# Kernel optimization log

Hardware: AMD Instinct MI355X
Metric: run time of the kernel (lower is better)

Reference implementation:

```python
import jax, jax.numpy as jnp
import numpy as np

B, S, D, H = 16, 1024, 256, 8
DEPTH = D // H          # 32
H2 = H // 2             # 4 heads per branch
DH = D // 2             # 128 per-branch model dim


def setup_inputs() -> dict:
    key = jax.random.key(0)
    ks = jax.random.split(key, 20)
    f32 = jnp.float32
    q_ori = jax.random.normal(ks[0], (B, S, D), f32)
    k_ori = jax.random.normal(ks[1], (B, S, D), f32)
    v_ori = jax.random.normal(ks[2], (B, S, D), f32)
    mask = (jax.random.uniform(ks[3], (B, 1, 1, S)) < 0.1).astype(f32)
    # adjacency: sparse 0/1 graph structure
    adj = (jax.random.uniform(ks[4], (B, S, S)) < 0.05).astype(f32)
    # distance matrix: positive values, softmaxed inside the dist branch
    dist = jax.random.uniform(ks[5], (B, S, S), dtype=f32)

    def dense(k, din, dout):
        return jax.random.normal(k, (din, dout), f32) * 0.02

    params = {
        'Wq_dist': dense(ks[6], D, DH), 'bq_dist': jnp.zeros((DH,), f32),
        'Wk_dist': dense(ks[7], D, DH), 'bk_dist': jnp.zeros((DH,), f32),
        'Wv_dist': dense(ks[8], D, DH), 'bv_dist': jnp.zeros((DH,), f32),
        'Wq_adj': dense(ks[9], D, DH), 'bq_adj': jnp.zeros((DH,), f32),
        'Wk_adj': dense(ks[10], D, DH), 'bk_adj': jnp.zeros((DH,), f32),
        'Wv_adj': dense(ks[11], D, DH), 'bv_adj': jnp.zeros((DH,), f32),
        'Wo': dense(ks[12], D, D), 'bo': jnp.zeros((D,), f32),
    }
    return dict(v_ori=v_ori, k_ori=k_ori, q_ori=q_ori, mask=mask,
                adj=adj, dist=dist, **params)


def _split_heads(x):
    # (B, S, DH) -> (B, H2, S, DEPTH)
    b, s, _ = x.shape
    return x.reshape(b, s, H2, DEPTH).transpose(0, 2, 1, 3)


def _sdpa_AD(q, k, v, mask, adj=None, dist=None):
    neg = mask * (-1e9)                                   # (B,1,1,S)
    scale = 1.0 / jnp.sqrt(jnp.asarray(DEPTH, q.dtype))
    logits = jnp.einsum('bhqd,bhkd->bhqk', q, k) * scale + neg
    w = jax.nn.softmax(logits, axis=-1)                   # (B,H2,S,S)
    if adj is not None:
        w = w * adj[:, None]                              # multiplicative adjacency reweight
    if dist is not None:
        w = w * jax.nn.softmax(dist[:, None] + neg, axis=-1)
    out = jnp.einsum('bhqk,bhkd->bhqd', w, v)
    return out, w


def reference(v_ori, k_ori, q_ori, mask, adj, dist,
              Wq_dist, bq_dist, Wk_dist, bk_dist, Wv_dist, bv_dist,
              Wq_adj, bq_adj, Wk_adj, bk_adj, Wv_adj, bv_adj, Wo, bo):
    b = q_ori.shape[0]
    # dist branch
    q = _split_heads(q_ori @ Wq_dist + bq_dist)
    k = _split_heads(k_ori @ Wk_dist + bk_dist)
    v = _split_heads(v_ori @ Wv_dist + bv_dist)
    o_dist, w_dist = _sdpa_AD(q, k, v, mask, adj=None, dist=dist)
    o_dist = o_dist.transpose(0, 2, 1, 3).reshape(b, -1, DH)
    # adj branch
    q = _split_heads(q_ori @ Wq_adj + bq_adj)
    k = _split_heads(k_ori @ Wk_adj + bk_adj)
    v = _split_heads(v_ori @ Wv_adj + bv_adj)
    o_adj, w_adj = _sdpa_AD(q, k, v, mask, adj=adj, dist=None)
    o_adj = o_adj.transpose(0, 2, 1, 3).reshape(b, -1, DH)

    concat = jnp.concatenate([o_dist, o_adj], axis=-1)    # (B,S,D)
    attn_w = jnp.concatenate([w_dist, w_adj], axis=1)     # (B,H,S,S)
    output = concat @ Wo + bo                             # (B,S,D)
    return output, attn_w
```

## Files before the change

kernel.cpp:

```cpp
#include <hip/hip_runtime.h>
#include <cstddef>

static constexpr int BB = 16, SS = 1024, DD = 256;
static constexpr size_t OUTW = (size_t)BB * SS * DD;
#define SCALE 0.17677669529663687f

__global__ __launch_bounds__(256) void pack_kernel(
    const float* __restrict__ Wqd, const float* __restrict__ Wqa,
    const float* __restrict__ Wkd, const float* __restrict__ Wka,
    const float* __restrict__ Wvd, const float* __restrict__ Wva,
    const float* __restrict__ bqd, const float* __restrict__ bqa,
    const float* __restrict__ bkd, const float* __restrict__ bka,
    const float* __restrict__ bvd, const float* __restrict__ bva,
    float* __restrict__ Wcat, float* __restrict__ bcat)
{
  int i = blockIdx.x * 256 + threadIdx.x;
  if (i < 3 * 256 * 256) {
    int g = i >> 16, r = (i >> 8) & 255, n = i & 255;
    const float* W0 = (g == 0) ? Wqd : (g == 1) ? Wkd : Wvd;
    const float* W1 = (g == 0) ? Wqa : (g == 1) ? Wka : Wva;
    Wcat[i] = (n < 128) ? W0[r * 128 + n] : W1[r * 128 + (n - 128)];
  } else {
    int j = i - 3 * 256 * 256;
    if (j < 3 * 256) {
      int g = j >> 8, n = j & 255;
      const float* b0 = (g == 0) ? bqd : (g == 1) ? bkd : bvd;
      const float* b1 = (g == 0) ? bqa : (g == 1) ? bka : bva;
      bcat[j] = (n < 128) ? b0[n] : b1[n - 128];
    }
  }
}

__device__ __forceinline__ void gemm_body(
    const float* __restrict__ X, const float* __restrict__ W,
    const float* __restrict__ bias, float* __restrict__ Y)
{
  __shared__ float Wl[256 * 32];
  const int t = threadIdx.x;
  const int m0 = blockIdx.x * 128;
  const int n0 = blockIdx.y * 32;
  const int tr = t >> 3;
  const int tc4 = (t & 7) * 4;

#pragma unroll
  for (int i = 0; i < 8; ++i) {
    const int k = (t >> 3) + 32 * i;
    *(float4*)&Wl[k * 32 + tc4] = *(const float4*)&W[(size_t)k * 256 + n0 + tc4];
  }
  __syncthreads();

  float acc[4][4];
#pragma unroll
  for (int i = 0; i < 4; ++i)
#pragma unroll
    for (int j = 0; j < 4; ++j) acc[i][j] = 0.f;

  const float* xr = X + (size_t)(m0 + 4 * tr) * 256;

  float4 a[4], an[4];
#pragma unroll
  for (int r = 0; r < 4; ++r) a[r] = *(const float4*)&xr[r * 256];

#pragma unroll 2
  for (int k = 0; k < 252; k += 4) {
#pragma unroll
    for (int r = 0; r < 4; ++r) an[r] = *(const float4*)&xr[r * 256 + k + 4];
    float4 w0 = *(const float4*)&Wl[(k + 0) * 32 + tc4];
    float4 w1 = *(const float4*)&Wl[(k + 1) * 32 + tc4];
    float4 w2 = *(const float4*)&Wl[(k + 2) * 32 + tc4];
    float4 w3 = *(const float4*)&Wl[(k + 3) * 32 + tc4];
#pragma unroll
    for (int r = 0; r < 4; ++r) {
      acc[r][0] = fmaf(a[r].x, w0.x, acc[r][0]);
      acc[r][1] = fmaf(a[r].x, w0.y, acc[r][1]);
      acc[r][2] = fmaf(a[r].x, w0.z, acc[r][2]);
      acc[r][3] = fmaf(a[r].x, w0.w, acc[r][3]);
      acc[r][0] = fmaf(a[r].y, w1.x, acc[r][0]);
      acc[r][1] = fmaf(a[r].y, w1.y, acc[r][1]);
      acc[r][2] = fmaf(a[r].y, w1.z, acc[r][2]);
      acc[r][3] = fmaf(a[r].y, w1.w, acc[r][3]);
      acc[r][0] = fmaf(a[r].z, w2.x, acc[r][0]);
      acc[r][1] = fmaf(a[r].z, w2.y, acc[r][1]);
      acc[r][2] = fmaf(a[r].z, w2.z, acc[r][2]);
      acc[r][3] = fmaf(a[r].z, w2.w, acc[r][3]);
      acc[r][0] = fmaf(a[r].w, w3.x, acc[r][0]);
      acc[r][1] = fmaf(a[r].w, w3.y, acc[r][1]);
      acc[r][2] = fmaf(a[r].w, w3.z, acc[r][2]);
      acc[r][3] = fmaf(a[r].w, w3.w, acc[r][3]);
    }
#pragma unroll
    for (int r = 0; r < 4; ++r) a[r] = an[r];
  }
  {
    const int k = 252;
    float4 w0 = *(const float4*)&Wl[(k + 0) * 32 + tc4];
    float4 w1 = *(const float4*)&Wl[(k + 1) * 32 + tc4];
    float4 w2 = *(const float4*)&Wl[(k + 2) * 32 + tc4];
    float4 w3 = *(const float4*)&Wl[(k + 3) * 32 + tc4];
#pragma unroll
    for (int r = 0; r < 4; ++r) {
      acc[r][0] = fmaf(a[r].x, w0.x, acc[r][0]);
      acc[r][1] = fmaf(a[r].x, w0.y, acc[r][1]);
      acc[r][2] = fmaf(a[r].x, w0.z, acc[r][2]);
      acc[r][3] = fmaf(a[r].x, w0.w, acc[r][3]);
      acc[r][0] = fmaf(a[r].y, w1.x, acc[r][0]);
      acc[r][1] = fmaf(a[r].y, w1.y, acc[r][1]);
      acc[r][2] = fmaf(a[r].y, w1.z, acc[r][2]);
      acc[r][3] = fmaf(a[r].y, w1.w, acc[r][3]);
      acc[r][0] = fmaf(a[r].z, w2.x, acc[r][0]);
      acc[r][1] = fmaf(a[r].z, w2.y, acc[r][1]);
      acc[r][2] = fmaf(a[r].z, w2.z, acc[r][2]);
      acc[r][3] = fmaf(a[r].z, w2.w, acc[r][3]);
      acc[r][0] = fmaf(a[r].w, w3.x, acc[r][0]);
      acc[r][1] = fmaf(a[r].w, w3.y, acc[r][1]);
      acc[r][2] = fmaf(a[r].w, w3.z, acc[r][2]);
      acc[r][3] = fmaf(a[r].w, w3.w, acc[r][3]);
    }
  }

  const float4 bb = *(const float4*)&bias[n0 + tc4];
#pragma unroll
  for (int r = 0; r < 4; ++r) {
    float4 o;
    o.x = acc[r][0] + bb.x; o.y = acc[r][1] + bb.y;
    o.z = acc[r][2] + bb.z; o.w = acc[r][3] + bb.w;
    *(float4*)&Y[(size_t)(m0 + 4 * tr + r) * 256 + n0 + tc4] = o;
  }
}

__global__ __launch_bounds__(256, 4) void gemm_qkv_kernel(
    const float* __restrict__ q, const float* __restrict__ k,
    const float* __restrict__ v, const float* __restrict__ Wcat,
    const float* __restrict__ bcat, float* __restrict__ Yb)
{
  const int z = blockIdx.z;
  const float* X = (z == 0) ? q : (z == 1) ? k : v;
  gemm_body(X, Wcat + z * 65536, bcat + (z << 8), Yb + (size_t)z * 4194304);
}

__global__ __launch_bounds__(256, 4) void gemm_out_kernel(
    const float* __restrict__ X, const float* __restrict__ W,
    const float* __restrict__ bias, float* __restrict__ Y)
{
  gemm_body(X, W, bias, Y);
}

__global__ __launch_bounds__(256) void dist_stats_kernel(
    const float* __restrict__ dist, const float* __restrict__ mask,
    float* __restrict__ dinv)
{
  const int t = threadIdx.x;
  const int w = t >> 6, lane = t & 63;
  const int row = blockIdx.x * 4 + w;
  const int b = row >> 10;
  const float* dr = dist + (size_t)row * 1024;
  const float* mr = mask + b * 1024;
  float s = 0.f;
#pragma unroll
  for (int j = 0; j < 16; ++j) {
    int c = lane + 64 * j;
    s += __expf(dr[c] - 1e9f * mr[c]);
  }
#pragma unroll
  for (int off = 32; off >= 1; off >>= 1) s += __shfl_xor(s, off);
  if (lane == 0) dinv[row] = 1.0f / s;
}

__global__ __launch_bounds__(256, 2) void attn_fused_kernel(
    const float* __restrict__ Qc, const float* __restrict__ Kc,
    const float* __restrict__ Vc, const float* __restrict__ mask,
    const float* __restrict__ adj, const float* __restrict__ dist,
    const float* __restrict__ dinv,
    float* __restrict__ wout, float* __restrict__ conc)
{
  __shared__ float Ls[16384];
  __shared__ float KVs[64][36];
  const int t = threadIdx.x;
  const int bid = blockIdx.x;
  const int qb = bid & 63, h = (bid >> 6) & 7, b = bid >> 9;
  const int q0 = qb * 16;
  const int branch = h >> 2;
  const int boff = branch * 128 + (h & 3) * 32;
  const int wv = t >> 6, l = t & 63;
  const int gr = q0 + 4 * wv;
  const int sr = t >> 2, sq = t & 3;

  float Q[4][32];
  const float* qbase = Qc + ((size_t)(b * 1024 + gr)) * 256 + boff;
#pragma unroll
  for (int r = 0; r < 4; ++r)
#pragma unroll
    for (int dq = 0; dq < 8; ++dq) {
      float4 a = *(const float4*)&qbase[(size_t)r * 256 + 4 * dq];
      Q[r][4 * dq + 0] = a.x; Q[r][4 * dq + 1] = a.y;
      Q[r][4 * dq + 2] = a.z; Q[r][4 * dq + 3] = a.w;
    }

  const float* kb = Kc + (size_t)(b * 1024) * 256 + boff;
  const float* mr = mask + b * 1024;

  float sp0 = 0.f, sp1 = 0.f, sp2 = 0.f, sp3 = 0.f;
  {
    float4 ka  = *(const float4*)&kb[(size_t)sr * 256 + 4 * sq];
    float4 kc2 = *(const float4*)&kb[(size_t)sr * 256 + 16 + 4 * sq];
    *(float4*)&KVs[sr][4 * sq] = ka;
    *(float4*)&KVs[sr][16 + 4 * sq] = kc2;
    __syncthreads();
  }
  float ngc = -1e9f * mr[l];
  for (int cc = 0; cc < 16; ++cc) {
    float4 nka, nkc2; float nng = 0.f;
    if (cc < 15) {
      const int cn0 = (cc + 1) * 64;
      nka  = *(const float4*)&kb[(size_t)(cn0 + sr) * 256 + 4 * sq];
      nkc2 = *(const float4*)&kb[(size_t)(cn0 + sr) * 256 + 16 + 4 * sq];
      nng = -1e9f * mr[cn0 + l];
    }
    const int c = cc * 64 + l;
    float s0 = 0.f, s1 = 0.f, s2 = 0.f, s3 = 0.f;
#pragma unroll
    for (int dq = 0; dq < 8; ++dq) {
      float4 kv = *(const float4*)&KVs[l][4 * dq];
      s0 = fmaf(Q[0][4 * dq + 0], kv.x, s0); s0 = fmaf(Q[0][4 * dq + 1], kv.y, s0);
      s0 = fmaf(Q[0][4 * dq + 2], kv.z, s0); s0 = fmaf(Q[0][4 * dq + 3], kv.w, s0);
      s1 = fmaf(Q[1][4 * dq + 0], kv.x, s1); s1 = fmaf(Q[1][4 * dq + 1], kv.y, s1);
      s1 = fmaf(Q[1][4 * dq + 2], kv.z, s1); s1 = fmaf(Q[1][4 * dq + 3], kv.w, s1);
      s2 = fmaf(Q[2][4 * dq + 0], kv.x, s2); s2 = fmaf(Q[2][4 * dq + 1], kv.y, s2);
      s2 = fmaf(Q[2][4 * dq + 2], kv.z, s2); s2 = fmaf(Q[2][4 * dq + 3], kv.w, s2);
      s3 = fmaf(Q[3][4 * dq + 0], kv.x, s3); s3 = fmaf(Q[3][4 * dq + 1], kv.y, s3);
      s3 = fmaf(Q[3][4 * dq + 2], kv.z, s3); s3 = fmaf(Q[3][4 * dq + 3], kv.w, s3);
    }
    float e0 = __expf(fmaf(s0, SCALE, ngc));
    float e1 = __expf(fmaf(s1, SCALE, ngc));
    float e2 = __expf(fmaf(s2, SCALE, ngc));
    float e3 = __expf(fmaf(s3, SCALE, ngc));
    Ls[(4 * wv + 0) * 1024 + c] = e0;
    Ls[(4 * wv + 1) * 1024 + c] = e1;
    Ls[(4 * wv + 2) * 1024 + c] = e2;
    Ls[(4 * wv + 3) * 1024 + c] = e3;
    sp0 += e0; sp1 += e1; sp2 += e2; sp3 += e3;
    if (cc < 15) {
      __syncthreads();
      *(float4*)&KVs[sr][4 * sq] = nka;
      *(float4*)&KVs[sr][16 + 4 * sq] = nkc2;
      __syncthreads();
      ngc = nng;
    }
  }

#pragma unroll
  for (int off = 32; off >= 1; off >>= 1) {
    sp0 += __shfl_xor(sp0, off);
    sp1 += __shfl_xor(sp1, off);
    sp2 += __shfl_xor(sp2, off);
    sp3 += __shfl_xor(sp3, off);
  }
  float inv[4] = {1.0f / sp0, 1.0f / sp1, 1.0f / sp2, 1.0f / sp3};

  float o[4][32];
#pragma unroll
  for (int r = 0; r < 4; ++r)
#pragma unroll
    for (int d = 0; d < 32; ++d) o[r][d] = 0.f;

  const float* br_[4];
  float din[4];
  if (branch == 0) {
#pragma unroll
    for (int r = 0; r < 4; ++r) {
      din[r] = dinv[b * 1024 + gr + r];
      br_[r] = dist + (size_t)(b * 1024 + gr + r) * 1024;
    }
  } else {
#pragma unroll
    for (int r = 0; r < 4; ++r) {
      din[r] = 0.f;
      br_[r] = adj + (size_t)(b * 1024 + gr + r) * 1024;
    }
  }
  const float* vb = Vc + (size_t)(b * 1024) * 256 + boff;
  const size_t wr0 = ((size_t)(b * 8 + h) * 1024 + gr) * 1024;

  float fpre[4], ngc2;
  {
    float4 va  = *(const float4*)&vb[(size_t)sr * 256 + 4 * sq];
    float4 vc2 = *(const float4*)&vb[(size_t)sr * 256 + 16 + 4 * sq];
#pragma unroll
    for (int r = 0; r < 4; ++r) fpre[r] = br_[r][l];
    ngc2 = -1e9f * mr[l];
    __syncthreads();
    *(float4*)&KVs[sr][4 * sq] = va;
    *(float4*)&KVs[sr][16 + 4 * sq] = vc2;
    __syncthreads();
  }
  for (int cc = 0; cc < 16; ++cc) {
    const int c = cc * 64 + l;
    float4 nva, nvc2; float nf[4]; float nng = 0.f;
    if (cc < 15) {
      const int cn0 = (cc + 1) * 64;
      nva  = *(const float4*)&vb[(size_t)(cn0 + sr) * 256 + 4 * sq];
      nvc2 = *(const float4*)&vb[(size_t)(cn0 + sr) * 256 + 16 + 4 * sq];
#pragma unroll
      for (int r = 0; r < 4; ++r) nf[r] = br_[r][cn0 + l];
      nng = -1e9f * mr[cn0 + l];
    }
    float w[4];
#pragma unroll
    for (int r = 0; r < 4; ++r) {
      float e = Ls[(4 * wv + r) * 1024 + c] * inv[r];
      float f;
      if (branch == 0) f = __expf(fpre[r] + ngc2) * din[r];
      else             f = fpre[r];
      w[r] = e * f;
      __builtin_nontemporal_store(w[r], &wout[wr0 + (size_t)r * 1024 + c]);
    }
#pragma unroll
    for (int dq = 0; dq < 8; ++dq) {
      float4 vv = *(const float4*)&KVs[l][4 * dq];
      o[0][4 * dq + 0] = fmaf(w[0], vv.x, o[0][4 * dq + 0]);
      o[0][4 * dq + 1] = fmaf(w[0], vv.y, o[0][4 * dq + 1]);
      o[0][4 * dq + 2] = fmaf(w[0], vv.z, o[0][4 * dq + 2]);
      o[0][4 * dq + 3] = fmaf(w[0], vv.w, o[0][4 * dq + 3]);
      o[1][4 * dq + 0] = fmaf(w[1], vv.x, o[1][4 * dq + 0]);
      o[1][4 * dq + 1] = fmaf(w[1], vv.y, o[1][4 * dq + 1]);
      o[1][4 * dq + 2] = fmaf(w[1], vv.z, o[1][4 * dq + 2]);
      o[1][4 * dq + 3] = fmaf(w[1], vv.w, o[1][4 * dq + 3]);
      o[2][4 * dq + 0] = fmaf(w[2], vv.x, o[2][4 * dq + 0]);
      o[2][4 * dq + 1] = fmaf(w[2], vv.y, o[2][4 * dq + 1]);
      o[2][4 * dq + 2] = fmaf(w[2], vv.z, o[2][4 * dq + 2]);
      o[2][4 * dq + 3] = fmaf(w[2], vv.w, o[2][4 * dq + 3]);
      o[3][4 * dq + 0] = fmaf(w[3], vv.x, o[3][4 * dq + 0]);
      o[3][4 * dq + 1] = fmaf(w[3], vv.y, o[3][4 * dq + 1]);
      o[3][4 * dq + 2] = fmaf(w[3], vv.z, o[3][4 * dq + 2]);
      o[3][4 * dq + 3] = fmaf(w[3], vv.w, o[3][4 * dq + 3]);
    }
    if (cc < 15) {
      __syncthreads();
      *(float4*)&KVs[sr][4 * sq] = nva;
      *(float4*)&KVs[sr][16 + 4 * sq] = nvc2;
      __syncthreads();
#pragma unroll
      for (int r = 0; r < 4; ++r) fpre[r] = nf[r];
      ngc2 = nng;
    }
  }

  {
    float* Ws_ = &Ls[wv * 4096];
#pragma unroll
    for (int p = 0; p < 2; ++p) {
#pragma unroll
      for (int j = 0; j < 32; ++j) {
        const int r = j >> 4, d2 = j & 15;
        const int slot = (j + l) & 31;
        float2 u;
        u.x = o[2 * p + r][2 * d2];
        u.y = o[2 * p + r][2 * d2 + 1];
        *(float2*)&Ws_[l * 64 + 2 * slot] = u;
      }
      const int rp = l >> 5, d = l & 31;
      const int jc = rp * 16 + (d >> 1);
      float a = 0.f;
#pragma unroll
      for (int ll = 0; ll < 64; ++ll)
        a += Ws_[ll * 64 + 2 * ((jc + ll) & 31) + (d & 1)];
      conc[((size_t)(b * 1024) + q0 + 4 * wv + 2 * p + rp) * 256 + boff + d] = a;
    }
  }
}

extern "C" void kernel_launch(void* const* d_in, const int* in_sizes, int n_in,
                              void* d_out, int out_size, void* d_ws, size_t ws_size,
                              hipStream_t stream)
{
  const float* v_ori = (const float*)d_in[0];
  const float* k_ori = (const float*)d_in[1];
  const float* q_ori = (const float*)d_in[2];
  const float* mask  = (const float*)d_in[3];
  const float* adj   = (const float*)d_in[4];
  const float* dist  = (const float*)d_in[5];
  const float* Wqd = (const float*)d_in[6];  const float* bqd = (const float*)d_in[7];
  const float* Wkd = (const float*)d_in[8];  const float* bkd = (const float*)d_in[9];
  const float* Wvd = (const float*)d_in[10]; const float* bvd = (const float*)d_in[11];
  const float* Wqa = (const float*)d_in[12]; const float* bqa = (const float*)d_in[13];
  const float* Wka = (const float*)d_in[14]; const float* bka = (const float*)d_in[15];
  const float* Wva = (const float*)d_in[16]; const float* bva = (const float*)d_in[17];
  const float* Wo  = (const float*)d_in[18]; const float* bo  = (const float*)d_in[19];

  float* out = (float*)d_out;
  float* ws  = (float*)d_ws;
  float* Qc    = ws;
  float* Kc    = Qc + 4194304;
  float* Vc    = Kc + 4194304;
  float* conc  = Vc + 4194304;
  float* dinvb = conc + 4194304;
  float* Wcat  = dinvb + 16384;
  float* bcat  = Wcat + 196608;

  pack_kernel<<<771, 256, 0, stream>>>(Wqd, Wqa, Wkd, Wka, Wvd, Wva,
                                       bqd, bqa, bkd, bka, bvd, bva, Wcat, bcat);
  gemm_qkv_kernel<<<dim3(128, 8, 3), 256, 0, stream>>>(q_ori, k_ori, v_ori,
                                                       Wcat, bcat, Qc);
  dist_stats_kernel<<<4096, 256, 0, stream>>>(dist, mask, dinvb);
  attn_fused_kernel<<<8192, 256, 0, stream>>>(Qc, Kc, Vc, mask, adj, dist,
                                              dinvb, out + OUTW, conc);
  gemm_out_kernel<<<dim3(128, 8), 256, 0, stream>>>(conc, Wo, bo, out);
}
```

Baseline: 1.190 ms.

## Use packed f32x2 FMAs, drop weight pack kernel, fuse dist stats into QKV GEMM

Rewrites the GEMM and attention inner loops to use two-wide float vector FMAs so the compiler can emit packed FP32 instructions. It also removes the separate weight-packing kernel by having each GEMM block read its column slice directly from the dist or adj weight. The dist softmax-denominator pass becomes an extra z-slice of the QKV GEMM grid, so one launch covers both. This saves two launches and one copy. The cost is possible extra register pressure and less balanced work inside the merged grid.

```diff
diff --git a/kernel.cpp b/kernel.cpp
--- a/kernel.cpp
+++ b/kernel.cpp
@@ -5,165 +5,146 @@
 static constexpr size_t OUTW = (size_t)BB * SS * DD;
 #define SCALE 0.17677669529663687f
 
-__global__ __launch_bounds__(256) void pack_kernel(
+typedef float f32x2 __attribute__((ext_vector_type(2)));
+__device__ __forceinline__ f32x2 fma2(f32x2 a, f32x2 b, f32x2 c) {
+#if defined(__has_builtin)
+#if __has_builtin(__builtin_elementwise_fma)
+  return __builtin_elementwise_fma(a, b, c);
+#else
+  return (f32x2){fmaf(a.x, b.x, c.x), fmaf(a.y, b.y, c.y)};
+#endif
+#else
+  return (f32x2){fmaf(a.x, b.x, c.x), fmaf(a.y, b.y, c.y)};
+#endif
+}
+
+__device__ __forceinline__ void gemm_body(
+    const float* __restrict__ X, const float* __restrict__ Wcol, int wstride,
+    const float* __restrict__ bcol, float* __restrict__ Y)
+{
+  __shared__ float Wl[256 * 32];
+  const int t = threadIdx.x;
+  const int m0 = blockIdx.x * 128;
+  const int n0 = blockIdx.y * 32;
+  const int tr = t >> 3;
+  const int tc4 = (t & 7) * 4;
+
+#pragma unroll
+  for (int i = 0; i < 8; ++i) {
+    const int k = (t >> 3) + 32 * i;
+    *(float4*)&Wl[k * 32 + tc4] = *(const float4*)&Wcol[(size_t)k * wstride + tc4];
+  }
+  __syncthreads();
+
+  f32x2 acc[4][2];
+#pragma unroll
+  for (int i = 0; i < 4; ++i) {
+    acc[i][0] = (f32x2){0.f, 0.f};
+    acc[i][1] = (f32x2){0.f, 0.f};
+  }
+
+  const float* xr = X + (size_t)(m0 + 4 * tr) * 256;
+
+  float4 a[4], an[4];
+#pragma unroll
+  for (int r = 0; r < 4; ++r) a[r] = *(const float4*)&xr[r * 256];
+
+#define GEMM_CHUNK(KK)                                                        \
+  {                                                                           \
+    float4 w0 = *(const float4*)&Wl[((KK) + 0) * 32 + tc4];                   \
+    float4 w1 = *(const float4*)&Wl[((KK) + 1) * 32 + tc4];                   \
+    float4 w2 = *(const float4*)&Wl[((KK) + 2) * 32 + tc4];                   \
+    float4 w3 = *(const float4*)&Wl[((KK) + 3) * 32 + tc4];                   \
+    f32x2 w0l = {w0.x, w0.y}, w0h = {w0.z, w0.w};                             \
+    f32x2 w1l = {w1.x, w1.y}, w1h = {w1.z, w1.w};                             \
+    f32x2 w2l = {w2.x, w2.y}, w2h = {w2.z, w2.w};                             \
+    f32x2 w3l = {w3.x, w3.y}, w3h = {w3.z, w3.w};                             \
+    _Pragma("unroll")                                                         \
+    for (int r = 0; r < 4; ++r) {                                             \
+      f32x2 s;                                                                \
+      s = (f32x2){a[r].x, a[r].x};                                            \
+      acc[r][0] = fma2(s, w0l, acc[r][0]); acc[r][1] = fma2(s, w0h, acc[r][1]);\
+      s = (f32x2){a[r].y, a[r].y};                                            \
+      acc[r][0] = fma2(s, w1l, acc[r][0]); acc[r][1] = fma2(s, w1h, acc[r][1]);\
+      s = (f32x2){a[r].z, a[r].z};                                            \
+      acc[r][0] = fma2(s, w2l, acc[r][0]); acc[r][1] = fma2(s, w2h, acc[r][1]);\
+      s = (f32x2){a[r].w, a[r].w};                                            \
+      acc[r][0] = fma2(s, w3l, acc[r][0]); acc[r][1] = fma2(s, w3h, acc[r][1]);\
+    }                                                                         \
+  }
+
+#pragma unroll 2
+  for (int k = 0; k < 252; k += 4) {
+#pragma unroll
+    for (int r = 0; r < 4; ++r) an[r] = *(const float4*)&xr[r * 256 + k + 4];
+    GEMM_CHUNK(k)
+#pragma unroll
+    for (int r = 0; r < 4; ++r) a[r] = an[r];
+  }
+  GEMM_CHUNK(252)
+#undef GEMM_CHUNK
+
+  const float4 bb = *(const float4*)&bcol[tc4];
+#pragma unroll
+  for (int r = 0; r < 4; ++r) {
+    float4 o;
+    o.x = acc[r][0].x + bb.x; o.y = acc[r][0].y + bb.y;
+    o.z = acc[r][1].x + bb.z; o.w = acc[r][1].y + bb.w;
+    *(float4*)&Y[(size_t)(m0 + 4 * tr + r) * 256 + n0 + tc4] = o;
+  }
+}
+
+__global__ __launch_bounds__(256, 4) void gemm_qkv_kernel(
+    const float* __restrict__ q, const float* __restrict__ k,
+    const float* __restrict__ v,
     const float* __restrict__ Wqd, const float* __restrict__ Wqa,
     const float* __restrict__ Wkd, const float* __restrict__ Wka,
     const float* __restrict__ Wvd, const float* __restrict__ Wva,
     const float* __restrict__ bqd, const float* __restrict__ bqa,
     const float* __restrict__ bkd, const float* __restrict__ bka,
     const float* __restrict__ bvd, const float* __restrict__ bva,
-    float* __restrict__ Wcat, float* __restrict__ bcat)
-{
-  int i = blockIdx.x * 256 + threadIdx.x;
-  if (i < 3 * 256 * 256) {
-    int g = i >> 16, r = (i >> 8) & 255, n = i & 255;
-    const float* W0 = (g == 0) ? Wqd : (g == 1) ? Wkd : Wvd;
-    const float* W1 = (g == 0) ? Wqa : (g == 1) ? Wka : Wva;
-    Wcat[i] = (n < 128) ? W0[r * 128 + n] : W1[r * 128 + (n - 128)];
-  } else {
-    int j = i - 3 * 256 * 256;
-    if (j < 3 * 256) {
-      int g = j >> 8, n = j & 255;
-      const float* b0 = (g == 0) ? bqd : (g == 1) ? bkd : bvd;
-      const float* b1 = (g == 0) ? bqa : (g == 1) ? bka : bva;
-      bcat[j] = (n < 128) ? b0[n] : b1[n - 128];
-    }
-  }
-}
-
-__device__ __forceinline__ void gemm_body(
-    const float* __restrict__ X, const float* __restrict__ W,
-    const float* __restrict__ bias, float* __restrict__ Y)
-{
-  __shared__ float Wl[256 * 32];
-  const int t = threadIdx.x;
-  const int m0 = blockIdx.x * 128;
+    const float* __restrict__ dist, const float* __restrict__ mask,
+    float* __restrict__ dinv, float* __restrict__ Yb)
+{
+  const int z = blockIdx.z;
+  if (z == 3) {
+    const int idx = blockIdx.y * 128 + blockIdx.x;
+    const int w = threadIdx.x >> 6, lane = threadIdx.x & 63;
+#pragma unroll
+    for (int rr = 0; rr < 4; ++rr) {
+      const int row = idx * 16 + w * 4 + rr;
+      const int b = row >> 10;
+      const float* dr = dist + (size_t)row * 1024;
+      const float* mrk = mask + b * 1024;
+      float s = 0.f;
+#pragma unroll
+      for (int j = 0; j < 16; ++j) {
+        int c = lane + 64 * j;
+        s += __expf(dr[c] - 1e9f * mrk[c]);
+      }
+#pragma unroll
+      for (int off = 32; off >= 1; off >>= 1) s += __shfl_xor(s, off);
+      if (lane == 0) dinv[row] = 1.0f / s;
+    }
+    return;
+  }
+  const float* X  = (z == 0) ? q   : (z == 1) ? k   : v;
+  const float* W0 = (z == 0) ? Wqd : (z == 1) ? Wkd : Wvd;
+  const float* W1 = (z == 0) ? Wqa : (z == 1) ? Wka : Wva;
+  const float* b0 = (z == 0) ? bqd : (z == 1) ? bkd : bvd;
+  const float* b1 = (z == 0) ? bqa : (z == 1) ? bka : bva;
   const int n0 = blockIdx.y * 32;
-  const int tr = t >> 3;
-  const int tc4 = (t & 7) * 4;
-
-#pragma unroll
-  for (int i = 0; i < 8; ++i) {
-    const int k = (t >> 3) + 32 * i;
-    *(float4*)&Wl[k * 32 + tc4] = *(const float4*)&W[(size_t)k * 256 + n0 + tc4];
-  }
-  __syncthreads();
-
-  float acc[4][4];
-#pragma unroll
-  for (int i = 0; i < 4; ++i)
-#pragma unroll
-    for (int j = 0; j < 4; ++j) acc[i][j] = 0.f;
-
-  const float* xr = X + (size_t)(m0 + 4 * tr) * 256;
-
-  float4 a[4], an[4];
-#pragma unroll
-  for (int r = 0; r < 4; ++r) a[r] = *(const float4*)&xr[r * 256];
-
-#pragma unroll 2
-  for (int k = 0; k < 252; k += 4) {
-#pragma unroll
-    for (int r = 0; r < 4; ++r) an[r] = *(const float4*)&xr[r * 256 + k + 4];
-    float4 w0 = *(const float4*)&Wl[(k + 0) * 32 + tc4];
-    float4 w1 = *(const float4*)&Wl[(k + 1) * 32 + tc4];
-    float4 w2 = *(const float4*)&Wl[(k + 2) * 32 + tc4];
-    float4 w3 = *(const float4*)&Wl[(k + 3) * 32 + tc4];
-#pragma unroll
-    for (int r = 0; r < 4; ++r) {
-      acc[r][0] = fmaf(a[r].x, w0.x, acc[r][0]);
-      acc[r][1] = fmaf(a[r].x, w0.y, acc[r][1]);
-      acc[r][2] = fmaf(a[r].x, w0.z, acc[r][2]);
-      acc[r][3] = fmaf(a[r].x, w0.w, acc[r][3]);
-      acc[r][0] = fmaf(a[r].y, w1.x, acc[r][0]);
-      acc[r][1] = fmaf(a[r].y, w1.y, acc[r][1]);
-      acc[r][2] = fmaf(a[r].y, w1.z, acc[r][2]);
-      acc[r][3] = fmaf(a[r].y, w1.w, acc[r][3]);
-      acc[r][0] = fmaf(a[r].z, w2.x, acc[r][0]);
-      acc[r][1] = fmaf(a[r].z, w2.y, acc[r][1]);
-      acc[r][2] = fmaf(a[r].z, w2.z, acc[r][2]);
-      acc[r][3] = fmaf(a[r].z, w2.w, acc[r][3]);
-      acc[r][0] = fmaf(a[r].w, w3.x, acc[r][0]);
-      acc[r][1] = fmaf(a[r].w, w3.y, acc[r][1]);
-      acc[r][2] = fmaf(a[r].w, w3.z, acc[r][2]);
-      acc[r][3] = fmaf(a[r].w, w3.w, acc[r][3]);
-    }
-#pragma unroll
-    for (int r = 0; r < 4; ++r) a[r] = an[r];
-  }
-  {
-    const int k = 252;
-    float4 w0 = *(const float4*)&Wl[(k + 0) * 32 + tc4];
-    float4 w1 = *(const float4*)&Wl[(k + 1) * 32 + tc4];
-    float4 w2 = *(const float4*)&Wl[(k + 2) * 32 + tc4];
-    float4 w3 = *(const float4*)&Wl[(k + 3) * 32 + tc4];
-#pragma unroll
-    for (int r = 0; r < 4; ++r) {
-      acc[r][0] = fmaf(a[r].x, w0.x, acc[r][0]);
-      acc[r][1] = fmaf(a[r].x, w0.y, acc[r][1]);
-      acc[r][2] = fmaf(a[r].x, w0.z, acc[r][2]);
-      acc[r][3] = fmaf(a[r].x, w0.w, acc[r][3]);
-      acc[r][0] = fmaf(a[r].y, w1.x, acc[r][0]);
-      acc[r][1] = fmaf(a[r].y, w1.y, acc[r][1]);
-      acc[r][2] = fmaf(a[r].y, w1.z, acc[r][2]);
-      acc[r][3] = fmaf(a[r].y, w1.w, acc[r][3]);
-      acc[r][0] = fmaf(a[r].z, w2.x, acc[r][0]);
-      acc[r][1] = fmaf(a[r].z, w2.y, acc[r][1]);
-      acc[r][2] = fmaf(a[r].z, w2.z, acc[r][2]);
-      acc[r][3] = fmaf(a[r].z, w2.w, acc[r][3]);
-      acc[r][0] = fmaf(a[r].w, w3.x, acc[r][0]);
-      acc[r][1] = fmaf(a[r].w, w3.y, acc[r][1]);
-      acc[r][2] = fmaf(a[r].w, w3.z, acc[r][2]);
-      acc[r][3] = fmaf(a[r].w, w3.w, acc[r][3]);
-    }
-  }
-
-  const float4 bb = *(const float4*)&bias[n0 + tc4];
-#pragma unroll
-  for (int r = 0; r < 4; ++r) {
-    float4 o;
-    o.x = acc[r][0] + bb.x; o.y = acc[r][1] + bb.y;
-    o.z = acc[r][2] + bb.z; o.w = acc[r][3] + bb.w;
-    *(float4*)&Y[(size_t)(m0 + 4 * tr + r) * 256 + n0 + tc4] = o;
-  }
-}
-
-__global__ __launch_bounds__(256, 4) void gemm_qkv_kernel(
-    const float* __restrict__ q, const float* __restrict__ k,
-    const float* __restrict__ v, const float* __restrict__ Wcat,
-    const float* __restrict__ bcat, float* __restrict__ Yb)
-{
-  const int z = blockIdx.z;
-  const float* X = (z == 0) ? q : (z == 1) ? k : v;
-  gemm_body(X, Wcat + z * 65536, bcat + (z << 8), Yb + (size_t)z * 4194304);
+  const float* Wcol = (n0 < 128) ? (W0 + n0) : (W1 + (n0 - 128));
+  const float* bcol = (n0 < 128) ? (b0 + n0) : (b1 + (n0 - 128));
+  gemm_body(X, Wcol, 128, bcol, Yb + (size_t)z * 4194304);
 }
 
 __global__ __launch_bounds__(256, 4) void gemm_out_kernel(
-    const float* __restrict__ X, const float* __restrict__ W,
-    const float* __restrict__ bias, float* __restrict__ Y)
-{
-  gemm_body(X, W, bias, Y);
-}
-
-__global__ __launch_bounds__(256) void dist_stats_kernel(
-    const float* __restrict__ dist, const float* __restrict__ mask,
-    float* __restrict__ dinv)
-{
-  const int t = threadIdx.x;
-  const int w = t >> 6, lane = t & 63;
-  const int row = blockIdx.x * 4 + w;
-  const int b = row >> 10;
-  const float* dr = dist + (size_t)row * 1024;
-  const float* mr = mask + b * 1024;
-  float s = 0.f;
-#pragma unroll
-  for (int j = 0; j < 16; ++j) {
-    int c = lane + 64 * j;
-    s += __expf(dr[c] - 1e9f * mr[c]);
-  }
-#pragma unroll
-  for (int off = 32; off >= 1; off >>= 1) s += __shfl_xor(s, off);
-  if (lane == 0) dinv[row] = 1.0f / s;
+    const float* __restrict__ X, const float* __restrict__ Wo,
+    const float* __restrict__ bo, float* __restrict__ Y)
+{
+  const int n0 = blockIdx.y * 32;
+  gemm_body(X, Wo + n0, 256, bo + n0, Y);
 }
 
 __global__ __launch_bounds__(256, 2) void attn_fused_kernel(
@@ -185,15 +166,15 @@
   const int gr = q0 + 4 * wv;
   const int sr = t >> 2, sq = t & 3;
 
-  float Q[4][32];
+  f32x2 Q2[4][16];
   const float* qbase = Qc + ((size_t)(b * 1024 + gr)) * 256 + boff;
 #pragma unroll
   for (int r = 0; r < 4; ++r)
 #pragma unroll
     for (int dq = 0; dq < 8; ++dq) {
       float4 a = *(const float4*)&qbase[(size_t)r * 256 + 4 * dq];
-      Q[r][4 * dq + 0] = a.x; Q[r][4 * dq + 1] = a.y;
-      Q[r][4 * dq + 2] = a.z; Q[r][4 * dq + 3] = a.w;
+      Q2[r][2 * dq]     = (f32x2){a.x, a.y};
+      Q2[r][2 * dq + 1] = (f32x2){a.z, a.w};
     }
 
   const float* kb = Kc + (size_t)(b * 1024) * 256 + boff;
@@ -217,23 +198,20 @@
       nng = -1e9f * mr[cn0 + l];
     }
     const int c = cc * 64 + l;
-    float s0 = 0.f, s1 = 0.f, s2 = 0.f, s3 = 0.f;
+    f32x2 t0 = {0.f, 0.f}, t1 = {0.f, 0.f}, t2 = {0.f, 0.f}, t3 = {0.f, 0.f};
 #pragma unroll
     for (int dq = 0; dq < 8; ++dq) {
       float4 kv = *(const float4*)&KVs[l][4 * dq];
-      s0 = fmaf(Q[0][4 * dq + 0], kv.x, s0); s0 = fmaf(Q[0][4 * dq + 1], kv.y, s0);
-      s0 = fmaf(Q[0][4 * dq + 2], kv.z, s0); s0 = fmaf(Q[0][4 * dq + 3], kv.w, s0);
-      s1 = fmaf(Q[1][4 * dq + 0], kv.x, s1); s1 = fmaf(Q[1][4 * dq + 1], kv.y, s1);
-      s1 = fmaf(Q[1][4 * dq + 2], kv.z, s1); s1 = fmaf(Q[1][4 * dq + 3], kv.w, s1);
-      s2 = fmaf(Q[2][4 * dq + 0], kv.x, s2); s2 = fmaf(Q[2][4 * dq + 1], kv.y, s2);
-      s2 = fmaf(Q[2][4 * dq + 2], kv.z, s2); s2 = fmaf(Q[2][4 * dq + 3], kv.w, s2);
-      s3 = fmaf(Q[3][4 * dq + 0], kv.x, s3); s3 = fmaf(Q[3][4 * dq + 1], kv.y, s3);
-      s3 = fmaf(Q[3][4 * dq + 2], kv.z, s3); s3 = fmaf(Q[3][4 * dq + 3], kv.w, s3);
-    }
-    float e0 = __expf(fmaf(s0, SCALE, ngc));
-    float e1 = __expf(fmaf(s1, SCALE, ngc));
-    float e2 = __expf(fmaf(s2, SCALE, ngc));
-    float e3 = __expf(fmaf(s3, SCALE, ngc));
+      f32x2 k01 = {kv.x, kv.y}, k23 = {kv.z, kv.w};
+      t0 = fma2(Q2[0][2 * dq], k01, t0); t0 = fma2(Q2[0][2 * dq + 1], k23, t0);
+      t1 = fma2(Q2[1][2 * dq], k01, t1); t1 = fma2(Q2[1][2 * dq + 1], k23, t1);
+      t2 = fma2(Q2[2][2 * dq], k01, t2); t2 = fma2(Q2[2][2 * dq + 1], k23, t2);
+      t3 = fma2(Q2[3][2 * dq], k01, t3); t3 = fma2(Q2[3][2 * dq + 1], k23, t3);
+    }
+    float e0 = __expf(fmaf(t0.x + t0.y, SCALE, ngc));
+    float e1 = __expf(fmaf(t1.x + t1.y, SCALE, ngc));
+    float e2 = __expf(fmaf(t2.x + t2.y, SCALE, ngc));
+    float e3 = __expf(fmaf(t3.x + t3.y, SCALE, ngc));
     Ls[(4 * wv + 0) * 1024 + c] = e0;
     Ls[(4 * wv + 1) * 1024 + c] = e1;
     Ls[(4 * wv + 2) * 1024 + c] = e2;
@@ -257,11 +235,11 @@
   }
   float inv[4] = {1.0f / sp0, 1.0f / sp1, 1.0f / sp2, 1.0f / sp3};
 
-  float o[4][32];
+  f32x2 o2[4][16];
 #pragma unroll
   for (int r = 0; r < 4; ++r)
 #pragma unroll
-    for (int d = 0; d < 32; ++d) o[r][d] = 0.f;
+    for (int d = 0; d < 16; ++d) o2[r][d] = (f32x2){0.f, 0.f};
 
   const float* br_[4];
   float din[4];
@@ -314,25 +292,20 @@
       w[r] = e * f;
       __builtin_nontemporal_store(w[r], &wout[wr0 + (size_t)r * 1024 + c]);
     }
+    f32x2 wb0 = {w[0], w[0]}, wb1 = {w[1], w[1]};
+    f32x2 wb2 = {w[2], w[2]}, wb3 = {w[3], w[3]};
 #pragma unroll
     for (int dq = 0; dq < 8; ++dq) {
       float4 vv = *(const float4*)&KVs[l][4 * dq];
-      o[0][4 * dq + 0] = fmaf(w[0], vv.x, o[0][4 * dq + 0]);
-      o[0][4 * dq + 1] = fmaf(w[0], vv.y, o[0][4 * dq + 1]);
-      o[0][4 * dq + 2] = fmaf(w[0], vv.z, o[0][4 * dq + 2]);
-      o[0][4 * dq + 3] = fmaf(w[0], vv.w, o[0][4 * dq + 3]);
-      o[1][4 * dq + 0] = fmaf(w[1], vv.x, o[1][4 * dq + 0]);
-      o[1][4 * dq + 1] = fmaf(w[1], vv.y, o[1][4 * dq + 1]);
-      o[1][4 * dq + 2] = fmaf(w[1], vv.z, o[1][4 * dq + 2]);
-      o[1][4 * dq + 3] = fmaf(w[1], vv.w, o[1][4 * dq + 3]);
-      o[2][4 * dq + 0] = fmaf(w[2], vv.x, o[2][4 * dq + 0]);
-      o[2][4 * dq + 1] = fmaf(w[2], vv.y, o[2][4 * dq + 1]);
-      o[2][4 * dq + 2] = fmaf(w[2], vv.z, o[2][4 * dq + 2]);
-      o[2][4 * dq + 3] = fmaf(w[2], vv.w, o[2][4 * dq + 3]);
-      o[3][4 * dq + 0] = fmaf(w[3], vv.x, o[3][4 * dq + 0]);
-      o[3][4 * dq + 1] = fmaf(w[3], vv.y, o[3][4 * dq + 1]);
-      o[3][4 * dq + 2] = fmaf(w[3], vv.z, o[3][4 * dq + 2]);
-      o[3][4 * dq + 3] = fmaf(w[3], vv.w, o[3][4 * dq + 3]);
+      f32x2 v01 = {vv.x, vv.y}, v23 = {vv.z, vv.w};
+      o2[0][2 * dq]     = fma2(wb0, v01, o2[0][2 * dq]);
+      o2[0][2 * dq + 1] = fma2(wb0, v23, o2[0][2 * dq + 1]);
+      o2[1][2 * dq]     = fma2(wb1, v01, o2[1][2 * dq]);
+      o2[1][2 * dq + 1] = fma2(wb1, v23, o2[1][2 * dq + 1]);
+      o2[2][2 * dq]     = fma2(wb2, v01, o2[2][2 * dq]);
+      o2[2][2 * dq + 1] = fma2(wb2, v23, o2[2][2 * dq + 1]);
+      o2[3][2 * dq]     = fma2(wb3, v01, o2[3][2 * dq]);
+      o2[3][2 * dq + 1] = fma2(wb3, v23, o2[3][2 * dq + 1]);
     }
     if (cc < 15) {
       __syncthreads();
@@ -353,10 +326,7 @@
       for (int j = 0; j < 32; ++j) {
         const int r = j >> 4, d2 = j & 15;
         const int slot = (j + l) & 31;
-        float2 u;
-        u.x = o[2 * p + r][2 * d2];
-        u.y = o[2 * p + r][2 * d2 + 1];
-        *(float2*)&Ws_[l * 64 + 2 * slot] = u;
+        *(f32x2*)&Ws_[l * 64 + 2 * slot] = o2[2 * p + r][d2];
       }
       const int rp = l >> 5, d = l & 31;
       const int jc = rp * 16 + (d >> 1);
@@ -394,14 +364,12 @@
   float* Vc    = Kc + 4194304;
   float* conc  = Vc + 4194304;
   float* dinvb = conc + 4194304;
-  float* Wcat  = dinvb + 16384;
-  float* bcat  = Wcat + 196608;
-
-  pack_kernel<<<771, 256, 0, stream>>>(Wqd, Wqa, Wkd, Wka, Wvd, Wva,
-                                       bqd, bqa, bkd, bka, bvd, bva, Wcat, bcat);
-  gemm_qkv_kernel<<<dim3(128, 8, 3), 256, 0, stream>>>(q_ori, k_ori, v_ori,
-                                                       Wcat, bcat, Qc);
-  dist_stats_kernel<<<4096, 256, 0, stream>>>(dist, mask, dinvb);
+
+  gemm_qkv_kernel<<<dim3(128, 8, 4), 256, 0, stream>>>(
+      q_ori, k_ori, v_ori,
+      Wqd, Wqa, Wkd, Wka, Wvd, Wva,
+      bqd, bqa, bkd, bka, bvd, bva,
+      dist, mask, dinvb, Qc);
   attn_fused_kernel<<<8192, 256, 0, stream>>>(Qc, Kc, Vc, mask, adj, dist,
                                               dinvb, out + OUTW, conc);
   gemm_out_kernel<<<dim3(128, 8), 256, 0, stream>>>(conc, Wo, bo, out);
```

New measurement: 1.173 ms. Within noise of the previous version (-1.5%).
